# Optimization experiments

Hardware: AMD Instinct MI355X
Metric: run time of the kernel (lower is better)

The kernel has to match this reference:

```python
import jax, jax.numpy as jnp
import numpy as np

B, N, M, D = 16, 128, 64, 512
H = 4
K = D // H  # head_dim = 128
L = 3      # num_labels


def setup_inputs() -> dict:
    key = jax.random.key(0)
    ks = jax.random.split(key, 16)
    s = 0.02
    return {
        "word": jax.random.normal(ks[0], (B, N, D), jnp.float32),
        "rel": jax.random.normal(ks[1], (B, M, D), jnp.float32),
        "mask": jnp.ones((B, M), jnp.float32),
        "Wn_w": jax.random.normal(ks[2], (D, D), jnp.float32) * s,
        "Wn_b": jnp.zeros((D,), jnp.float32),
        "Wr_w": jax.random.normal(ks[3], (D, D), jnp.float32) * s,
        "Wr_b": jnp.zeros((D,), jnp.float32),
        "lin_w": jax.random.normal(ks[4], (H, D, K), jnp.float32) * s,
        "lin_b": jnp.zeros((H, K), jnp.float32),
        "score_w": jax.random.normal(ks[5], (H, K), jnp.float32) * s,
        "score_b": jnp.zeros((H,), jnp.float32),
        "final_w": jax.random.normal(ks[6], (D, D), jnp.float32) * s,
        "final_b": jnp.zeros((D,), jnp.float32),
        "fc_w": jax.random.normal(ks[7], (D, L), jnp.float32) * s,
        "fc_b": jnp.zeros((L,), jnp.float32),
    }


def reference(word, rel, mask, Wn_w, Wn_b, Wr_w, Wr_b, lin_w, lin_b,
              score_w, score_b, final_w, final_b, fc_w, fc_b):
    # projections (dropout = identity in eval mode)
    w = word @ Wn_w + Wn_b                     # [B,N,D]
    r = rel @ Wr_w + Wr_b                      # [B,M,D]
    # outer-product hadamard + relu            # [B,N,M,D]
    had = jax.nn.relu(w[:, :, None, :] * r[:, None, :, :])
    # per-head linear projection, vectorized over heads
    t = jnp.einsum('bnmd,hdk->bnmhk', had, lin_w) + lin_b  # [B,N,M,H,K]
    # per-head scalar score + softmax over M (the dim=-1 of [B,N,M])
    s = jnp.einsum('bnmhk,hk->bnmh', t, score_w) + score_b  # [B,N,M,H]
    wts = jax.nn.softmax(s, axis=2) * mask[:, None, :, None]
    # masked weighted sum over M, then mean over N
    head = jnp.einsum('bnmh,bnmhk->bnhk', wts, t)           # [B,N,H,K]
    head = head.mean(axis=1).reshape(head.shape[0], H * K)  # [B,D] (concat heads)
    out = head @ final_w + final_b
    out = jax.nn.relu(out)
    logits = out @ fc_w + fc_b                               # [B,L]
    return logits
```

## Files before the change

### kernel.cpp

```cpp
#include <hip/hip_runtime.h>
#include <math.h>


#define OFF_W   0
#define OFF_R   (2048*512)
#define OFF_V   (OFF_R + 1024*512)
#define OFF_S   (OFF_V + 2048)
#define OFF_G   (OFF_S + 64*8192)
#define OFF_SW  (OFF_G + 64*512)
#define OFF_HM  (OFF_SW + 256)

__global__ __launch_bounds__(256) void proj_gemm(
    const float* __restrict__ word, const float* __restrict__ rel,
    const float* __restrict__ Wn_w, const float* __restrict__ Wn_b,
    const float* __restrict__ Wr_w, const float* __restrict__ Wr_b,
    const float* __restrict__ lin_w, const float* __restrict__ score_w,
    float* __restrict__ ws)
{
    int blk = blockIdx.x;
    if (blk >= 384) {
        int gid = (blk - 384) * 256 + threadIdx.x;
        int h = gid >> 9, d = gid & 511;
        const float* lw = lin_w + (size_t)(h * 512 + d) * 128;
        const float* sw = score_w + h * 128;
        float acc = 0.f;
        #pragma unroll 4
        for (int k = 0; k < 128; k += 4) {
            float4 a = *(const float4*)(lw + k);
            float4 b = *(const float4*)(sw + k);
            acc = fmaf(a.x, b.x, acc); acc = fmaf(a.y, b.y, acc);
            acc = fmaf(a.z, b.z, acc); acc = fmaf(a.w, b.w, acc);
        }
        ws[OFF_V + h * 512 + d] = 0.5f * acc;
        return;
    }
    const float *A, *W, *bias;
    float* C;
    int rowTile, colTile;
    if (blk < 256) {
        A = word; W = Wn_w; bias = Wn_b; C = ws + OFF_W;
        rowTile = blk >> 3; colTile = blk & 7;
    } else {
        int b2 = blk - 256;
        A = rel; W = Wr_w; bias = Wr_b; C = ws + OFF_R;
        rowTile = b2 >> 3; colTile = b2 & 7;
    }
    const int row0 = rowTile * 64, col0 = colTile * 64;

    __shared__ float As[16][68];
    __shared__ float Bs[16][64];

    const int t  = threadIdx.x;
    const int tx = t & 15, ty = t >> 4;
    const int lr = t >> 2, lk = (t & 3) << 2;
    const int bk = t >> 4, bc = (t & 15) << 2;

    float acc[4][4] = {};

    for (int k0 = 0; k0 < 512; k0 += 16) {
        float4 a4 = *(const float4*)(A + (size_t)(row0 + lr) * 512 + k0 + lk);
        As[lk + 0][lr] = a4.x; As[lk + 1][lr] = a4.y;
        As[lk + 2][lr] = a4.z; As[lk + 3][lr] = a4.w;
        *(float4*)&Bs[bk][bc] = *(const float4*)(W + (size_t)(k0 + bk) * 512 + col0 + bc);
        __syncthreads();
        #pragma unroll
        for (int kk = 0; kk < 16; kk++) {
            float4 av = *(float4*)&As[kk][ty << 2];
            float4 bv = *(float4*)&Bs[kk][tx << 2];
            float aa[4] = {av.x, av.y, av.z, av.w};
            float bb[4] = {bv.x, bv.y, bv.z, bv.w};
            #pragma unroll
            for (int i = 0; i < 4; i++)
                #pragma unroll
                for (int j = 0; j < 4; j++)
                    acc[i][j] = fmaf(aa[i], bb[j], acc[i][j]);
        }
        __syncthreads();
    }
    float4 bv = *(const float4*)(bias + col0 + (tx << 2));
    float bb[4] = {bv.x, bv.y, bv.z, bv.w};
    #pragma unroll
    for (int i = 0; i < 4; i++) {
        float4 o;
        o.x = acc[i][0] + bb[0]; o.y = acc[i][1] + bb[1];
        o.z = acc[i][2] + bb[2]; o.w = acc[i][3] + bb[3];
        *(float4*)(C + (size_t)(row0 + (ty << 2) + i) * 512 + col0 + (tx << 2)) = o;
    }
}

__global__ __launch_bounds__(256) void scores_sm(
    const float* __restrict__ mask, float* __restrict__ ws)
{
    const int blk = blockIdx.x;
    const int nq = blk & 3, bh = blk >> 2, h = bh & 3, b = bh >> 2;
    const int n0 = nq * 32;

    const float* wbase = ws + OFF_W + (size_t)(b * 128) * 512;
    const float* rbase = ws + OFF_R + (size_t)(b * 64) * 512;
    float* wtsT = ws + OFF_S + (size_t)bh * 8192;

    __shared__ float v2s[512];
    __shared__ float maskl[64];
    __shared__ float Arv[2][16][68];
    __shared__ float Ara[2][16][68];
    __shared__ float Wl[2][16][36];
    __shared__ float sl[64][33];
    __shared__ float pmax[8][33], psum[8][33], pms[8][33];

    const int t = threadIdx.x;
    if (t < 128) *(float4*)&v2s[t * 4] = *(const float4*)(ws + OFF_V + h * 512 + t * 4);
    if (t < 64) maskl[t] = mask[b * 64 + t];

    const int tm = t & 15, tn = t >> 4;
    const int sm = t >> 2, sk = (t & 3) * 4;
    const int wn = t >> 2, wk = (t & 3) * 4;
    __syncthreads();

    {
        float4 r4 = *(const float4*)(rbase + (size_t)sm * 512 + sk);
        float4 vv = *(const float4*)&v2s[sk];
        Arv[0][sk + 0][sm] = r4.x * vv.x; Ara[0][sk + 0][sm] = fabsf(r4.x) * vv.x;
        Arv[0][sk + 1][sm] = r4.y * vv.y; Ara[0][sk + 1][sm] = fabsf(r4.y) * vv.y;
        Arv[0][sk + 2][sm] = r4.z * vv.z; Ara[0][sk + 2][sm] = fabsf(r4.z) * vv.z;
        Arv[0][sk + 3][sm] = r4.w * vv.w; Ara[0][sk + 3][sm] = fabsf(r4.w) * vv.w;
        if (t < 128) {
            float4 w4 = *(const float4*)(wbase + (size_t)(n0 + wn) * 512 + wk);
            Wl[0][wk + 0][wn] = w4.x; Wl[0][wk + 1][wn] = w4.y;
            Wl[0][wk + 2][wn] = w4.z; Wl[0][wk + 3][wn] = w4.w;
        }
    }
    __syncthreads();

    float acc[4][2] = {};
    int buf = 0;
    for (int s = 0; s < 32; s++) {
        float4 r4n, w4n;
        const int k0n = (s + 1) * 16;
        if (s < 31) {
            r4n = *(const float4*)(rbase + (size_t)sm * 512 + k0n + sk);
            if (t < 128)
                w4n = *(const float4*)(wbase + (size_t)(n0 + wn) * 512 + k0n + wk);
        }
        #pragma unroll
        for (int kk = 0; kk < 16; kk++) {
            float4 rv = *(float4*)&Arv[buf][kk][tm * 4];
            float4 ra = *(float4*)&Ara[buf][kk][tm * 4];
            float2 wv = *(float2*)&Wl[buf][kk][tn * 2];
            float wax = fabsf(wv.x), way = fabsf(wv.y);
            acc[0][0] = fmaf(rv.x, wv.x, acc[0][0]); acc[0][0] = fmaf(ra.x, wax, acc[0][0]);
            acc[1][0] = fmaf(rv.y, wv.x, acc[1][0]); acc[1][0] = fmaf(ra.y, wax, acc[1][0]);
            acc[2][0] = fmaf(rv.z, wv.x, acc[2][0]); acc[2][0] = fmaf(ra.z, wax, acc[2][0]);
            acc[3][0] = fmaf(rv.w, wv.x, acc[3][0]); acc[3][0] = fmaf(ra.w, wax, acc[3][0]);
            acc[0][1] = fmaf(rv.x, wv.y, acc[0][1]); acc[0][1] = fmaf(ra.x, way, acc[0][1]);
            acc[1][1] = fmaf(rv.y, wv.y, acc[1][1]); acc[1][1] = fmaf(ra.y, way, acc[1][1]);
            acc[2][1] = fmaf(rv.z, wv.y, acc[2][1]); acc[2][1] = fmaf(ra.z, way, acc[2][1]);
            acc[3][1] = fmaf(rv.w, wv.y, acc[3][1]); acc[3][1] = fmaf(ra.w, way, acc[3][1]);
        }
        if (s < 31) {
            float4 vv = *(const float4*)&v2s[k0n + sk];
            const int nb = buf ^ 1;
            Arv[nb][sk + 0][sm] = r4n.x * vv.x; Ara[nb][sk + 0][sm] = fabsf(r4n.x) * vv.x;
            Arv[nb][sk + 1][sm] = r4n.y * vv.y; Ara[nb][sk + 1][sm] = fabsf(r4n.y) * vv.y;
            Arv[nb][sk + 2][sm] = r4n.z * vv.z; Ara[nb][sk + 2][sm] = fabsf(r4n.z) * vv.z;
            Arv[nb][sk + 3][sm] = r4n.w * vv.w; Ara[nb][sk + 3][sm] = fabsf(r4n.w) * vv.w;
            if (t < 128) {
                Wl[nb][wk + 0][wn] = w4n.x; Wl[nb][wk + 1][wn] = w4n.y;
                Wl[nb][wk + 2][wn] = w4n.z; Wl[nb][wk + 3][wn] = w4n.w;
            }
        }
        __syncthreads();
        buf ^= 1;
    }

    #pragma unroll
    for (int i = 0; i < 4; i++) {
        sl[tm * 4 + i][tn * 2 + 0] = acc[i][0];
        sl[tm * 4 + i][tn * 2 + 1] = acc[i][1];
    }
    __syncthreads();

    const int col = t & 31, seg = t >> 5;
    {
        float mx = sl[seg * 8 + 0][col];
        #pragma unroll
        for (int q = 1; q < 8; q++) mx = fmaxf(mx, sl[seg * 8 + q][col]);
        pmax[seg][col] = mx;
    }
    __syncthreads();
    float gmx = pmax[0][col];
    #pragma unroll
    for (int q = 1; q < 8; q++) gmx = fmaxf(gmx, pmax[q][col]);
    float es[8], ps = 0.f, pm = 0.f;
    #pragma unroll
    for (int q = 0; q < 8; q++) {
        int m = seg * 8 + q;
        float e = expf(sl[m][col] - gmx);
        es[q] = e; ps += e; pm = fmaf(e, maskl[m], pm);
    }
    psum[seg][col] = ps; pms[seg][col] = pm;
    __syncthreads();
    float tot = psum[0][col];
    #pragma unroll
    for (int q = 1; q < 8; q++) tot += psum[q][col];
    const float inv = 1.0f / tot;
    float o[8];
    #pragma unroll
    for (int q = 0; q < 8; q++) o[q] = es[q] * inv * maskl[seg * 8 + q];
    float4 o0; o0.x = o[0]; o0.y = o[1]; o0.z = o[2]; o0.w = o[3];
    float4 o1; o1.x = o[4]; o1.y = o[5]; o1.z = o[6]; o1.w = o[7];
    *(float4*)(wtsT + (size_t)(n0 + col) * 64 + seg * 8)     = o0;
    *(float4*)(wtsT + (size_t)(n0 + col) * 64 + seg * 8 + 4) = o1;
    if (seg == 0) {
        float pmt = pms[0][col];
        #pragma unroll
        for (int q = 1; q < 8; q++) pmt += pms[q][col];
        float swc = pmt * inv;
        #pragma unroll
        for (int off = 16; off > 0; off >>= 1)
            swc += __shfl_xor(swc, off);
        if (col == 0) ws[OFF_SW + bh * 4 + nq] = swc;
    }
}

__global__ __launch_bounds__(256) void gstep_kernel(float* __restrict__ ws)
{
    const int blk = blockIdx.x;
    const int dtile = blk & 7, bh = blk >> 3;
    const int b = bh >> 2;
    const int d0 = dtile * 64;
    const float* wtsT  = ws + OFF_S + (size_t)bh * 8192;
    const float* wbase = ws + OFF_W + (size_t)(b * 128) * 512;
    const float* rbase = ws + OFF_R + (size_t)(b * 64) * 512;

    __shared__ float As[16][68];
    __shared__ float Bs[16][68];
    __shared__ float Ba[16][68];
    __shared__ float red[16][68];

    const int t = threadIdx.x;
    const int tx = t & 15, ty = t >> 4;
    const int an_r = t >> 4, am4 = (t & 15) * 4;
    const int bn = t >> 4, bd4 = (t & 15) * 4;

    float accC[4][4] = {}, accA[4][4] = {};

    for (int n0 = 0; n0 < 128; n0 += 16) {
        *(float4*)&As[an_r][am4] =
            *(const float4*)(wtsT + (size_t)(n0 + an_r) * 64 + am4);
        float4 b4 = *(const float4*)(wbase + (size_t)(n0 + bn) * 512 + d0 + bd4);
        *(float4*)&Bs[bn][bd4] = b4;
        float4 bb; bb.x = fabsf(b4.x); bb.y = fabsf(b4.y);
        bb.z = fabsf(b4.z); bb.w = fabsf(b4.w);
        *(float4*)&Ba[bn][bd4] = bb;
        __syncthreads();
        #pragma unroll
        for (int kk = 0; kk < 16; kk++) {
            float4 av  = *(float4*)&As[kk][ty * 4];
            float4 bv  = *(float4*)&Bs[kk][tx * 4];
            float4 bav = *(float4*)&Ba[kk][tx * 4];
            float av_[4]  = {av.x, av.y, av.z, av.w};
            float bv_[4]  = {bv.x, bv.y, bv.z, bv.w};
            float bav_[4] = {bav.x, bav.y, bav.z, bav.w};
            #pragma unroll
            for (int i = 0; i < 4; i++)
                #pragma unroll
                for (int j = 0; j < 4; j++) {
                    accC[i][j] = fmaf(av_[i], bv_[j],  accC[i][j]);
                    accA[i][j] = fmaf(av_[i], bav_[j], accA[i][j]);
                }
        }
        __syncthreads();
    }
    float g0 = 0.f, g1 = 0.f, g2 = 0.f, g3 = 0.f;
    #pragma unroll
    for (int i = 0; i < 4; i++) {
        float4 rv = *(const float4*)(rbase + (size_t)(ty * 4 + i) * 512 + d0 + tx * 4);
        g0 = fmaf(rv.x, accC[i][0], g0); g0 = fmaf(fabsf(rv.x), accA[i][0], g0);
        g1 = fmaf(rv.y, accC[i][1], g1); g1 = fmaf(fabsf(rv.y), accA[i][1], g1);
        g2 = fmaf(rv.z, accC[i][2], g2); g2 = fmaf(fabsf(rv.z), accA[i][2], g2);
        g3 = fmaf(rv.w, accC[i][3], g3); g3 = fmaf(fabsf(rv.w), accA[i][3], g3);
    }
    float4 gg; gg.x = g0; gg.y = g1; gg.z = g2; gg.w = g3;
    *(float4*)&red[ty][tx * 4] = gg;
    __syncthreads();
    if (t < 64) {
        float s = 0.f;
        #pragma unroll
        for (int q = 0; q < 16; q++) s += red[q][t];
        ws[OFF_G + (size_t)bh * 512 + d0 + t] = 0.5f * s;
    }
}

__global__ __launch_bounds__(256) void headmean_kernel(
    const float* __restrict__ lin_w, const float* __restrict__ lin_b,
    float* __restrict__ ws)
{
    const int blk = blockIdx.x;
    const int kt = blk & 3, bh = blk >> 2, b = bh >> 2, h = bh & 3;
    const int t = threadIdx.x;
    const int dg = t >> 5, kk = t & 31;
    const int k = kt * 32 + kk;

    __shared__ float Gs[512];
    __shared__ float red[8][33];

    Gs[t]       = ws[OFF_G + (size_t)bh * 512 + t];
    Gs[t + 256] = ws[OFF_G + (size_t)bh * 512 + t + 256];
    __syncthreads();

    const float* lwp = lin_w + ((size_t)h * 512 + dg * 64) * 128 + k;
    const float* gp = Gs + dg * 64;
    float acc = 0.f;
    #pragma unroll 8
    for (int d = 0; d < 64; d++)
        acc = fmaf(gp[d], lwp[(size_t)d * 128], acc);
    red[dg][kk] = acc;
    __syncthreads();
    if (t < 32) {
        float s = 0.f;
        #pragma unroll
        for (int q = 0; q < 8; q++) s += red[q][t];
        const float SWv = ws[OFF_SW + bh * 4 + 0] + ws[OFF_SW + bh * 4 + 1]
                        + ws[OFF_SW + bh * 4 + 2] + ws[OFF_SW + bh * 4 + 3];
        s = fmaf(lin_b[h * 128 + kt * 32 + t], SWv, s);
        ws[OFF_HM + (size_t)b * 512 + h * 128 + kt * 32 + t] = s * (1.0f / 128.0f);
    }
}

__global__ __launch_bounds__(256) void final_logits(
    const float* __restrict__ final_w, const float* __restrict__ final_b,
    const float* __restrict__ fc_w, const float* __restrict__ fc_b,
    const float* __restrict__ ws, float* __restrict__ out)
{
    const int blk = blockIdx.x;
    const int jt = blk & 15, b = blk >> 4;
    const int t = threadIdx.x;
    const int dg = t >> 5, jj = t & 31;
    const int j = jt * 32 + jj;

    __shared__ float hs[512];
    __shared__ float red[8][33];
    __shared__ float osl[32];

    hs[t]       = ws[OFF_HM + (size_t)b * 512 + t];
    hs[t + 256] = ws[OFF_HM + (size_t)b * 512 + t + 256];
    __syncthreads();

    const float* fwp = final_w + (size_t)(dg * 64) * 512 + j;
    const float* hp = hs + dg * 64;
    float acc = 0.f;
    #pragma unroll 8
    for (int d = 0; d < 64; d++)
        acc = fmaf(hp[d], fwp[(size_t)d * 512], acc);
    red[dg][jj] = acc;
    __syncthreads();
    if (t < 32) {
        float s = 0.f;
        #pragma unroll
        for (int q = 0; q < 8; q++) s += red[q][t];
        osl[t] = fmaxf(s + final_b[jt * 32 + t], 0.f);
    }
    __syncthreads();
    if (t < 96) {
        const int l = t >> 5, j2 = t & 31;
        float val = osl[j2] * fc_w[(jt * 32 + j2) * 3 + l];
        #pragma unroll
        for (int off = 16; off > 0; off >>= 1)
            val += __shfl_xor(val, off);
        if (j2 == 0) atomicAdd(out + b * 3 + l, val);
    }
    if (jt == 0 && t < 3) atomicAdd(out + b * 3 + t, fc_b[t]);
}

extern "C" void kernel_launch(void* const* d_in, const int* in_sizes, int n_in,
                              void* d_out, int out_size, void* d_ws, size_t ws_size,
                              hipStream_t stream)
{
    const float* word    = (const float*)d_in[0];
    const float* rel     = (const float*)d_in[1];
    const float* mask    = (const float*)d_in[2];
    const float* Wn_w    = (const float*)d_in[3];
    const float* Wn_b    = (const float*)d_in[4];
    const float* Wr_w    = (const float*)d_in[5];
    const float* Wr_b    = (const float*)d_in[6];
    const float* lin_w   = (const float*)d_in[7];
    const float* lin_b   = (const float*)d_in[8];
    const float* score_w = (const float*)d_in[9];
    const float* final_w = (const float*)d_in[11];
    const float* final_b = (const float*)d_in[12];
    const float* fc_w    = (const float*)d_in[13];
    const float* fc_b    = (const float*)d_in[14];
    float* ws  = (float*)d_ws;
    float* out = (float*)d_out;

    hipMemsetAsync(out, 0, 16 * 3 * sizeof(float), stream);

    proj_gemm<<<392, 256, 0, stream>>>(word, rel, Wn_w, Wn_b, Wr_w, Wr_b,
                                       lin_w, score_w, ws);
    scores_sm<<<256, 256, 0, stream>>>(mask, ws);
    gstep_kernel<<<512, 256, 0, stream>>>(ws);
    headmean_kernel<<<256, 256, 0, stream>>>(lin_w, lin_b, ws);
    final_logits<<<256, 256, 0, stream>>>(final_w, final_b, fc_w, fc_b, ws, out);
}
```

Baseline: 182.6 us.

## Fuse headmean into gstep, enlarge projection tiles, double-buffer GEMMs, drop memset

The projection GEMM now uses 128x64 tiles with double-buffered shared memory, which halves the block count. The out zeroing moves into that kernel, so the hipMemsetAsync call is gone. The scores kernel drops its separate abs(r)*v shared buffer and rebuilds the term from |rv| and a copysign of w with v. gstep is double-buffered, computes |b| in registers, and absorbs the headmean projection by accumulating partial results with atomicAdd into a buffer that the scores kernel zeroes. This removes one launch plus several shared-memory loads and stores, at the cost of atomics and a larger register footprint.

```diff
diff --git a/kernel.cpp b/kernel.cpp
--- a/kernel.cpp
+++ b/kernel.cpp
@@ -15,11 +15,13 @@
     const float* __restrict__ Wn_w, const float* __restrict__ Wn_b,
     const float* __restrict__ Wr_w, const float* __restrict__ Wr_b,
     const float* __restrict__ lin_w, const float* __restrict__ score_w,
-    float* __restrict__ ws)
+    float* __restrict__ ws, float* __restrict__ out)
 {
-    int blk = blockIdx.x;
-    if (blk >= 384) {
-        int gid = (blk - 384) * 256 + threadIdx.x;
+    const int blk = blockIdx.x;
+    const int t = threadIdx.x;
+    if (blk >= 192) {
+        if (blk == 192 && t < 48) out[t] = 0.f;
+        int gid = (blk - 192) * 256 + t;
         int h = gid >> 9, d = gid & 511;
         const float* lw = lin_w + (size_t)(h * 512 + d) * 128;
         const float* sw = score_w + h * 128;
@@ -37,54 +39,76 @@
     const float *A, *W, *bias;
     float* C;
     int rowTile, colTile;
-    if (blk < 256) {
+    if (blk < 128) {
         A = word; W = Wn_w; bias = Wn_b; C = ws + OFF_W;
         rowTile = blk >> 3; colTile = blk & 7;
     } else {
-        int b2 = blk - 256;
+        int b2 = blk - 128;
         A = rel; W = Wr_w; bias = Wr_b; C = ws + OFF_R;
         rowTile = b2 >> 3; colTile = b2 & 7;
     }
-    const int row0 = rowTile * 64, col0 = colTile * 64;
-
-    __shared__ float As[16][68];
-    __shared__ float Bs[16][64];
-
-    const int t  = threadIdx.x;
+    const int row0 = rowTile * 128, col0 = colTile * 64;
+
+    __shared__ float As[2][16][132];
+    __shared__ float Bs[2][16][68];
+
     const int tx = t & 15, ty = t >> 4;
-    const int lr = t >> 2, lk = (t & 3) << 2;
-    const int bk = t >> 4, bc = (t & 15) << 2;
-
-    float acc[4][4] = {};
-
-    for (int k0 = 0; k0 < 512; k0 += 16) {
-        float4 a4 = *(const float4*)(A + (size_t)(row0 + lr) * 512 + k0 + lk);
-        As[lk + 0][lr] = a4.x; As[lk + 1][lr] = a4.y;
-        As[lk + 2][lr] = a4.z; As[lk + 3][lr] = a4.w;
-        *(float4*)&Bs[bk][bc] = *(const float4*)(W + (size_t)(k0 + bk) * 512 + col0 + bc);
-        __syncthreads();
+    const int ar = t >> 1, ks = (t & 1) * 8;
+    const int bk = t >> 4, bc = (t & 15) * 4;
+
+    float acc[8][4] = {};
+
+    {
+        float4 aA = *(const float4*)(A + (size_t)(row0 + ar) * 512 + ks);
+        float4 aB = *(const float4*)(A + (size_t)(row0 + ar) * 512 + ks + 4);
+        As[0][ks + 0][ar] = aA.x; As[0][ks + 1][ar] = aA.y;
+        As[0][ks + 2][ar] = aA.z; As[0][ks + 3][ar] = aA.w;
+        As[0][ks + 4][ar] = aB.x; As[0][ks + 5][ar] = aB.y;
+        As[0][ks + 6][ar] = aB.z; As[0][ks + 7][ar] = aB.w;
+        *(float4*)&Bs[0][bk][bc] = *(const float4*)(W + (size_t)bk * 512 + col0 + bc);
+    }
+    __syncthreads();
+
+    int buf = 0;
+    for (int s = 0; s < 32; s++) {
+        float4 aAn, aBn, bn4;
+        if (s < 31) {
+            const int k0n = (s + 1) * 16;
+            aAn = *(const float4*)(A + (size_t)(row0 + ar) * 512 + k0n + ks);
+            aBn = *(const float4*)(A + (size_t)(row0 + ar) * 512 + k0n + ks + 4);
+            bn4 = *(const float4*)(W + (size_t)(k0n + bk) * 512 + col0 + bc);
+        }
         #pragma unroll
         for (int kk = 0; kk < 16; kk++) {
-            float4 av = *(float4*)&As[kk][ty << 2];
-            float4 bv = *(float4*)&Bs[kk][tx << 2];
-            float aa[4] = {av.x, av.y, av.z, av.w};
+            float4 a0 = *(float4*)&As[buf][kk][ty * 8];
+            float4 a1 = *(float4*)&As[buf][kk][ty * 8 + 4];
+            float4 bv = *(float4*)&Bs[buf][kk][tx * 4];
+            float am[8] = {a0.x, a0.y, a0.z, a0.w, a1.x, a1.y, a1.z, a1.w};
             float bb[4] = {bv.x, bv.y, bv.z, bv.w};
             #pragma unroll
-            for (int i = 0; i < 4; i++)
+            for (int i = 0; i < 8; i++)
                 #pragma unroll
                 for (int j = 0; j < 4; j++)
-                    acc[i][j] = fmaf(aa[i], bb[j], acc[i][j]);
+                    acc[i][j] = fmaf(am[i], bb[j], acc[i][j]);
+        }
+        if (s < 31) {
+            const int nb = buf ^ 1;
+            As[nb][ks + 0][ar] = aAn.x; As[nb][ks + 1][ar] = aAn.y;
+            As[nb][ks + 2][ar] = aAn.z; As[nb][ks + 3][ar] = aAn.w;
+            As[nb][ks + 4][ar] = aBn.x; As[nb][ks + 5][ar] = aBn.y;
+            As[nb][ks + 6][ar] = aBn.z; As[nb][ks + 7][ar] = aBn.w;
+            *(float4*)&Bs[nb][bk][bc] = bn4;
         }
         __syncthreads();
-    }
-    float4 bv = *(const float4*)(bias + col0 + (tx << 2));
-    float bb[4] = {bv.x, bv.y, bv.z, bv.w};
-    #pragma unroll
-    for (int i = 0; i < 4; i++) {
+        buf ^= 1;
+    }
+    float4 bv4 = *(const float4*)(bias + col0 + tx * 4);
+    #pragma unroll
+    for (int i = 0; i < 8; i++) {
         float4 o;
-        o.x = acc[i][0] + bb[0]; o.y = acc[i][1] + bb[1];
-        o.z = acc[i][2] + bb[2]; o.w = acc[i][3] + bb[3];
-        *(float4*)(C + (size_t)(row0 + (ty << 2) + i) * 512 + col0 + (tx << 2)) = o;
+        o.x = acc[i][0] + bv4.x; o.y = acc[i][1] + bv4.y;
+        o.z = acc[i][2] + bv4.z; o.w = acc[i][3] + bv4.w;
+        *(float4*)(C + (size_t)(row0 + ty * 8 + i) * 512 + col0 + tx * 4) = o;
     }
 }
 
@@ -102,7 +126,6 @@
     __shared__ float v2s[512];
     __shared__ float maskl[64];
     __shared__ float Arv[2][16][68];
-    __shared__ float Ara[2][16][68];
     __shared__ float Wl[2][16][36];
     __shared__ float sl[64][33];
     __shared__ float pmax[8][33], psum[8][33], pms[8][33];
@@ -110,6 +133,7 @@
     const int t = threadIdx.x;
     if (t < 128) *(float4*)&v2s[t * 4] = *(const float4*)(ws + OFF_V + h * 512 + t * 4);
     if (t < 64) maskl[t] = mask[b * 64 + t];
+    if (t < 32) ws[OFF_HM + (size_t)b * 512 + h * 128 + n0 + t] = 0.f;
 
     const int tm = t & 15, tn = t >> 4;
     const int sm = t >> 2, sk = (t & 3) * 4;
@@ -119,10 +143,10 @@
     {
         float4 r4 = *(const float4*)(rbase + (size_t)sm * 512 + sk);
         float4 vv = *(const float4*)&v2s[sk];
-        Arv[0][sk + 0][sm] = r4.x * vv.x; Ara[0][sk + 0][sm] = fabsf(r4.x) * vv.x;
-        Arv[0][sk + 1][sm] = r4.y * vv.y; Ara[0][sk + 1][sm] = fabsf(r4.y) * vv.y;
-        Arv[0][sk + 2][sm] = r4.z * vv.z; Ara[0][sk + 2][sm] = fabsf(r4.z) * vv.z;
-        Arv[0][sk + 3][sm] = r4.w * vv.w; Ara[0][sk + 3][sm] = fabsf(r4.w) * vv.w;
+        Arv[0][sk + 0][sm] = r4.x * vv.x;
+        Arv[0][sk + 1][sm] = r4.y * vv.y;
+        Arv[0][sk + 2][sm] = r4.z * vv.z;
+        Arv[0][sk + 3][sm] = r4.w * vv.w;
         if (t < 128) {
             float4 w4 = *(const float4*)(wbase + (size_t)(n0 + wn) * 512 + wk);
             Wl[0][wk + 0][wn] = w4.x; Wl[0][wk + 1][wn] = w4.y;
@@ -144,25 +168,27 @@
         #pragma unroll
         for (int kk = 0; kk < 16; kk++) {
             float4 rv = *(float4*)&Arv[buf][kk][tm * 4];
-            float4 ra = *(float4*)&Ara[buf][kk][tm * 4];
             float2 wv = *(float2*)&Wl[buf][kk][tn * 2];
-            float wax = fabsf(wv.x), way = fabsf(wv.y);
-            acc[0][0] = fmaf(rv.x, wv.x, acc[0][0]); acc[0][0] = fmaf(ra.x, wax, acc[0][0]);
-            acc[1][0] = fmaf(rv.y, wv.x, acc[1][0]); acc[1][0] = fmaf(ra.y, wax, acc[1][0]);
-            acc[2][0] = fmaf(rv.z, wv.x, acc[2][0]); acc[2][0] = fmaf(ra.z, wax, acc[2][0]);
-            acc[3][0] = fmaf(rv.w, wv.x, acc[3][0]); acc[3][0] = fmaf(ra.w, wax, acc[3][0]);
-            acc[0][1] = fmaf(rv.x, wv.y, acc[0][1]); acc[0][1] = fmaf(ra.x, way, acc[0][1]);
-            acc[1][1] = fmaf(rv.y, wv.y, acc[1][1]); acc[1][1] = fmaf(ra.y, way, acc[1][1]);
-            acc[2][1] = fmaf(rv.z, wv.y, acc[2][1]); acc[2][1] = fmaf(ra.z, way, acc[2][1]);
-            acc[3][1] = fmaf(rv.w, wv.y, acc[3][1]); acc[3][1] = fmaf(ra.w, way, acc[3][1]);
+            float sv = v2s[s * 16 + kk];
+            float wax = copysignf(wv.x, sv), way = copysignf(wv.y, sv);
+            float r0 = fabsf(rv.x), r1 = fabsf(rv.y);
+            float r2 = fabsf(rv.z), r3 = fabsf(rv.w);
+            acc[0][0] = fmaf(rv.x, wv.x, acc[0][0]); acc[0][0] = fmaf(r0, wax, acc[0][0]);
+            acc[1][0] = fmaf(rv.y, wv.x, acc[1][0]); acc[1][0] = fmaf(r1, wax, acc[1][0]);
+            acc[2][0] = fmaf(rv.z, wv.x, acc[2][0]); acc[2][0] = fmaf(r2, wax, acc[2][0]);
+            acc[3][0] = fmaf(rv.w, wv.x, acc[3][0]); acc[3][0] = fmaf(r3, wax, acc[3][0]);
+            acc[0][1] = fmaf(rv.x, wv.y, acc[0][1]); acc[0][1] = fmaf(r0, way, acc[0][1]);
+            acc[1][1] = fmaf(rv.y, wv.y, acc[1][1]); acc[1][1] = fmaf(r1, way, acc[1][1]);
+            acc[2][1] = fmaf(rv.z, wv.y, acc[2][1]); acc[2][1] = fmaf(r2, way, acc[2][1]);
+            acc[3][1] = fmaf(rv.w, wv.y, acc[3][1]); acc[3][1] = fmaf(r3, way, acc[3][1]);
         }
         if (s < 31) {
             float4 vv = *(const float4*)&v2s[k0n + sk];
             const int nb = buf ^ 1;
-            Arv[nb][sk + 0][sm] = r4n.x * vv.x; Ara[nb][sk + 0][sm] = fabsf(r4n.x) * vv.x;
-            Arv[nb][sk + 1][sm] = r4n.y * vv.y; Ara[nb][sk + 1][sm] = fabsf(r4n.y) * vv.y;
-            Arv[nb][sk + 2][sm] = r4n.z * vv.z; Ara[nb][sk + 2][sm] = fabsf(r4n.z) * vv.z;
-            Arv[nb][sk + 3][sm] = r4n.w * vv.w; Ara[nb][sk + 3][sm] = fabsf(r4n.w) * vv.w;
+            Arv[nb][sk + 0][sm] = r4n.x * vv.x;
+            Arv[nb][sk + 1][sm] = r4n.y * vv.y;
+            Arv[nb][sk + 2][sm] = r4n.z * vv.z;
+            Arv[nb][sk + 3][sm] = r4n.w * vv.w;
             if (t < 128) {
                 Wl[nb][wk + 0][wn] = w4n.x; Wl[nb][wk + 1][wn] = w4n.y;
                 Wl[nb][wk + 2][wn] = w4n.z; Wl[nb][wk + 3][wn] = w4n.w;
@@ -222,20 +248,23 @@
     }
 }
 
-__global__ __launch_bounds__(256) void gstep_kernel(float* __restrict__ ws)
+__global__ __launch_bounds__(256) void gstep_kernel(
+    const float* __restrict__ lin_w, const float* __restrict__ lin_b,
+    float* __restrict__ ws)
 {
     const int blk = blockIdx.x;
     const int dtile = blk & 7, bh = blk >> 3;
-    const int b = bh >> 2;
+    const int b = bh >> 2, h = bh & 3;
     const int d0 = dtile * 64;
     const float* wtsT  = ws + OFF_S + (size_t)bh * 8192;
     const float* wbase = ws + OFF_W + (size_t)(b * 128) * 512;
     const float* rbase = ws + OFF_R + (size_t)(b * 64) * 512;
 
-    __shared__ float As[16][68];
-    __shared__ float Bs[16][68];
-    __shared__ float Ba[16][68];
+    __shared__ float As[2][16][68];
+    __shared__ float Bs[2][16][68];
     __shared__ float red[16][68];
+    __shared__ float Gs[64];
+    __shared__ float red2[128];
 
     const int t = threadIdx.x;
     const int tx = t & 15, ty = t >> 4;
@@ -244,32 +273,40 @@
 
     float accC[4][4] = {}, accA[4][4] = {};
 
-    for (int n0 = 0; n0 < 128; n0 += 16) {
-        *(float4*)&As[an_r][am4] =
-            *(const float4*)(wtsT + (size_t)(n0 + an_r) * 64 + am4);
-        float4 b4 = *(const float4*)(wbase + (size_t)(n0 + bn) * 512 + d0 + bd4);
-        *(float4*)&Bs[bn][bd4] = b4;
-        float4 bb; bb.x = fabsf(b4.x); bb.y = fabsf(b4.y);
-        bb.z = fabsf(b4.z); bb.w = fabsf(b4.w);
-        *(float4*)&Ba[bn][bd4] = bb;
-        __syncthreads();
+    *(float4*)&As[0][an_r][am4] = *(const float4*)(wtsT + (size_t)an_r * 64 + am4);
+    *(float4*)&Bs[0][bn][bd4]   = *(const float4*)(wbase + (size_t)bn * 512 + d0 + bd4);
+    __syncthreads();
+
+    int buf = 0;
+    for (int s = 0; s < 8; s++) {
+        float4 a4n, b4n;
+        if (s < 7) {
+            const int n0n = (s + 1) * 16;
+            a4n = *(const float4*)(wtsT + (size_t)(n0n + an_r) * 64 + am4);
+            b4n = *(const float4*)(wbase + (size_t)(n0n + bn) * 512 + d0 + bd4);
+        }
         #pragma unroll
         for (int kk = 0; kk < 16; kk++) {
-            float4 av  = *(float4*)&As[kk][ty * 4];
-            float4 bv  = *(float4*)&Bs[kk][tx * 4];
-            float4 bav = *(float4*)&Ba[kk][tx * 4];
-            float av_[4]  = {av.x, av.y, av.z, av.w};
-            float bv_[4]  = {bv.x, bv.y, bv.z, bv.w};
-            float bav_[4] = {bav.x, bav.y, bav.z, bav.w};
+            float4 av = *(float4*)&As[buf][kk][ty * 4];
+            float4 bv = *(float4*)&Bs[buf][kk][tx * 4];
+            float av_[4] = {av.x, av.y, av.z, av.w};
+            float bv_[4] = {bv.x, bv.y, bv.z, bv.w};
+            float ba_[4] = {fabsf(bv.x), fabsf(bv.y), fabsf(bv.z), fabsf(bv.w)};
             #pragma unroll
             for (int i = 0; i < 4; i++)
                 #pragma unroll
                 for (int j = 0; j < 4; j++) {
-                    accC[i][j] = fmaf(av_[i], bv_[j],  accC[i][j]);
-                    accA[i][j] = fmaf(av_[i], bav_[j], accA[i][j]);
+                    accC[i][j] = fmaf(av_[i], bv_[j], accC[i][j]);
+                    accA[i][j] = fmaf(av_[i], ba_[j], accA[i][j]);
                 }
         }
+        if (s < 7) {
+            const int nb = buf ^ 1;
+            *(float4*)&As[nb][an_r][am4] = a4n;
+            *(float4*)&Bs[nb][bn][bd4]   = b4n;
+        }
         __syncthreads();
+        buf ^= 1;
     }
     float g0 = 0.f, g1 = 0.f, g2 = 0.f, g3 = 0.f;
     #pragma unroll
@@ -287,43 +324,27 @@
         float s = 0.f;
         #pragma unroll
         for (int q = 0; q < 16; q++) s += red[q][t];
-        ws[OFF_G + (size_t)bh * 512 + d0 + t] = 0.5f * s;
-    }
-}
-
-__global__ __launch_bounds__(256) void headmean_kernel(
-    const float* __restrict__ lin_w, const float* __restrict__ lin_b,
-    float* __restrict__ ws)
-{
-    const int blk = blockIdx.x;
-    const int kt = blk & 3, bh = blk >> 2, b = bh >> 2, h = bh & 3;
-    const int t = threadIdx.x;
-    const int dg = t >> 5, kk = t & 31;
-    const int k = kt * 32 + kk;
-
-    __shared__ float Gs[512];
-    __shared__ float red[8][33];
-
-    Gs[t]       = ws[OFF_G + (size_t)bh * 512 + t];
-    Gs[t + 256] = ws[OFF_G + (size_t)bh * 512 + t + 256];
-    __syncthreads();
-
-    const float* lwp = lin_w + ((size_t)h * 512 + dg * 64) * 128 + k;
-    const float* gp = Gs + dg * 64;
-    float acc = 0.f;
+        Gs[t] = 0.5f * s;
+    }
+    __syncthreads();
+
+    const int k = t & 127, dh = t >> 7;
+    const float* lwp = lin_w + ((size_t)h * 512 + d0 + dh * 32) * 128 + k;
+    const float* gp = Gs + dh * 32;
+    float acc2 = 0.f;
     #pragma unroll 8
-    for (int d = 0; d < 64; d++)
-        acc = fmaf(gp[d], lwp[(size_t)d * 128], acc);
-    red[dg][kk] = acc;
-    __syncthreads();
-    if (t < 32) {
-        float s = 0.f;
-        #pragma unroll
-        for (int q = 0; q < 8; q++) s += red[q][t];
-        const float SWv = ws[OFF_SW + bh * 4 + 0] + ws[OFF_SW + bh * 4 + 1]
-                        + ws[OFF_SW + bh * 4 + 2] + ws[OFF_SW + bh * 4 + 3];
-        s = fmaf(lin_b[h * 128 + kt * 32 + t], SWv, s);
-        ws[OFF_HM + (size_t)b * 512 + h * 128 + kt * 32 + t] = s * (1.0f / 128.0f);
+    for (int d = 0; d < 32; d++)
+        acc2 = fmaf(gp[d], lwp[(size_t)d * 128], acc2);
+    if (dh) red2[k] = acc2;
+    __syncthreads();
+    if (!dh) {
+        float p = acc2 + red2[k];
+        if (dtile == 0) {
+            const float SWv = ws[OFF_SW + bh * 4 + 0] + ws[OFF_SW + bh * 4 + 1]
+                            + ws[OFF_SW + bh * 4 + 2] + ws[OFF_SW + bh * 4 + 3];
+            p = fmaf(lin_b[h * 128 + k], SWv, p);
+        }
+        atomicAdd(&ws[OFF_HM + (size_t)b * 512 + h * 128 + k], p * (1.0f / 128.0f));
     }
 }
 
@@ -393,12 +414,9 @@
     float* ws  = (float*)d_ws;
     float* out = (float*)d_out;
 
-    hipMemsetAsync(out, 0, 16 * 3 * sizeof(float), stream);
-
-    proj_gemm<<<392, 256, 0, stream>>>(word, rel, Wn_w, Wn_b, Wr_w, Wr_b,
-                                       lin_w, score_w, ws);
+    proj_gemm<<<200, 256, 0, stream>>>(word, rel, Wn_w, Wn_b, Wr_w, Wr_b,
+                                       lin_w, score_w, ws, out);
     scores_sm<<<256, 256, 0, stream>>>(mask, ws);
-    gstep_kernel<<<512, 256, 0, stream>>>(ws);
-    headmean_kernel<<<256, 256, 0, stream>>>(lin_w, lin_b, ws);
+    gstep_kernel<<<512, 256, 0, stream>>>(lin_w, lin_b, ws);
     final_logits<<<256, 256, 0, stream>>>(final_w, final_b, fc_w, fc_b, ws, out);
 }
```

After: 173.0 us. -5.3%, faster.
